# Performance work log

Measured on AMD Instinct MI355X. Metric: run time of the kernel, lower is better.

## Reference

```python
import jax, jax.numpy as jnp
import numpy as np


def _grid_sample_2d(feat, gx, gy):
    """Bilinear grid sample, zeros padding, align_corners=False.
    feat: [B,C,H,W]; gx,gy: [B,S,h,w] normalized coords in [-1,1].
    Returns [B,C,S,h,w]. Matches torch 5D grid_sample with D=1, z=0
    (z pixel coord = (1*1-1)/2 = 0 -> weight 1 on the single depth slice).
    """
    B, C, H, W = feat.shape
    ix = ((gx + 1.0) * W - 1.0) * 0.5  # unnormalize, align_corners=False
    iy = ((gy + 1.0) * H - 1.0) * 0.5
    x0 = jnp.floor(ix)
    y0 = jnp.floor(iy)
    tx = ix - x0  # fractional parts (differentiable w.r.t. grid)
    ty = iy - y0
    x0i = x0.astype(jnp.int32)
    y0i = y0.astype(jnp.int32)
    feat_flat = feat.reshape(B, C, H * W)

    def gather(xi, yi):
        valid = (xi >= 0) & (xi < W) & (yi >= 0) & (yi < H)
        xc = jnp.clip(xi, 0, W - 1)
        yc = jnp.clip(yi, 0, H - 1)
        idx = (yc * W + xc).reshape(B, 1, -1)  # [B,1,S*h*w]
        g = jnp.take_along_axis(feat_flat, idx, axis=2)  # [B,C,S*h*w]
        g = g.reshape(B, C, *xi.shape[1:])  # [B,C,S,h,w]
        return g * valid.astype(feat.dtype)[:, None]

    v00 = gather(x0i, y0i)
    v01 = gather(x0i + 1, y0i)
    v10 = gather(x0i, y0i + 1)
    v11 = gather(x0i + 1, y0i + 1)
    w00 = ((1.0 - tx) * (1.0 - ty))[:, None]
    w01 = (tx * (1.0 - ty))[:, None]
    w10 = ((1.0 - tx) * ty)[:, None]
    w11 = (tx * ty)[:, None]
    return v00 * w00 + v01 * w01 + v10 * w10 + v11 * w11


def setup_inputs() -> dict:
    key = jax.random.key(0)
    k1, k2, k3, k4 = jax.random.split(key, 4)
    B, C, S, H, W = 8, 8, 16, 128, 416
    feat_l = jax.random.normal(k1, (B, C, H, W), dtype=jnp.float32)
    feat_r = jax.random.normal(k2, (B, C, H, W), dtype=jnp.float32)
    # LUT: x,y normalized coords (slightly beyond [-1,1] to exercise zero padding);
    # z channel fixed to 0 exactly as in the module's lut_batch construction.
    lut_xy = jax.random.uniform(k3, (B, S, H, W, 2), dtype=jnp.float32,
                                minval=-1.1, maxval=1.1)
    lut = jnp.concatenate([lut_xy, jnp.zeros((B, S, H, W, 1), jnp.float32)], axis=-1)
    valid_mask = jax.random.bernoulli(k4, 0.8, (B, C, S, H, W))
    return {"feat_l": feat_l, "feat_r": feat_r, "lut": lut,
            "valid_mask": valid_mask, "no_steps": S}


def reference(feat_l, feat_r, lut, valid_mask, no_steps):
    """AnyNet._build_volume_2d: LUT grid_sample warp + masked inf-fill
    + abs-diff + channel-sum cost volume. Returns [B, no_steps, H, W]."""
    gx = lut[..., 0]  # torch grid order: (x, y, z), x indexes width
    gy = lut[..., 1]
    warped = _grid_sample_2d(feat_r, gx, gy)          # [B,C,S,H,W]
    diff = jnp.abs(warped - feat_l[:, :, None])       # broadcast feat_l over S
    cost_disp_feat = jnp.where(valid_mask, diff, jnp.inf)
    cost_volume = jnp.sum(cost_disp_feat, axis=1)     # [B,S,H,W]
    return cost_volume
```

## Files before the change

kernel.cpp:

```cpp
#include <hip/hip_runtime.h>
#include <math.h>

#define BB 8
#define CC 8
#define SS 16
#define HH 128
#define WW 416
#define HWSZ (HH * WW)

typedef unsigned short u16;
typedef unsigned char  u8;
typedef unsigned int   u32;
typedef unsigned short ushort8 __attribute__((ext_vector_type(8)));
typedef unsigned int   u32x4   __attribute__((ext_vector_type(4)));

__device__ __forceinline__ float bf2f(u16 v) {
    union { unsigned int u; float f; } x;
    x.u = ((unsigned int)v) << 16;
    return x.f;
}

__device__ __forceinline__ u16 f2bf(float f) {
    union { float ff; unsigned int u; } x;
    x.ff = f;
    unsigned int lsb = (x.u >> 16) & 1u;
    return (u16)((x.u + 0x7FFFu + lsb) >> 16);
}

__device__ __forceinline__ u32 nz_flags(u32 w) {
    return (((w & 0x7F7F7F7Fu) + 0x7F7F7F7Fu) | w) & 0x80808080u;
}

__global__ __launch_bounds__(256) void pack_feats(
    const u16* __restrict__ feat_l,
    const u16* __restrict__ feat_r,
    ushort8* __restrict__ pl,
    ushort8* __restrict__ pr)
{
    const int idx = blockIdx.x * 256 + threadIdx.x;
    const int b = idx / HWSZ;
    const int p = idx - b * HWSZ;
    const size_t base = (size_t)b * CC * HWSZ + p;

    ushort8 vr, vl;
#pragma unroll
    for (int c = 0; c < CC; ++c) {
        vr[c] = __builtin_nontemporal_load(&feat_r[base + (size_t)c * HWSZ]);
        vl[c] = __builtin_nontemporal_load(&feat_l[base + (size_t)c * HWSZ]);
    }
    pr[idx] = vr;
    pl[idx] = vl;
}

__global__ __launch_bounds__(256) void mask_reduce(
    const u8* __restrict__ vmask,
    u8* __restrict__ pmask)
{
    const int t = blockIdx.x * 256 + threadIdx.x;
    const int n16 = SS * HWSZ / 16;
    const int b = t / n16;
    const int r = t - b * n16;
    const u32x4* __restrict__ vm4 = (const u32x4*)vmask;

    u32x4 f = { 0x80808080u, 0x80808080u, 0x80808080u, 0x80808080u };
#pragma unroll
    for (int c = 0; c < CC; ++c) {
        const u32x4 v = __builtin_nontemporal_load(
            &vm4[(size_t)(b * CC + c) * n16 + r]);
        f.x &= nz_flags(v.x);
        f.y &= nz_flags(v.y);
        f.z &= nz_flags(v.z);
        f.w &= nz_flags(v.w);
    }
    __builtin_nontemporal_store(f, &((u32x4*)pmask)[t]);
}

__global__ __launch_bounds__(256) void anynet_cost_volume(
    const ushort8* __restrict__ pfr,
    const ushort8* __restrict__ pfl,
    const u16* __restrict__ lut,
    const u8*  __restrict__ pmask,
    u16* __restrict__ out)
{
    const int hw = blockIdx.x * 256 + threadIdx.x;
    const int bs = blockIdx.y;
    const int b  = bs >> 4;

    const size_t loff = ((size_t)bs * HWSZ + hw) * 3;
    const float gx = bf2f(__builtin_nontemporal_load(&lut[loff + 0]));
    const float gy = bf2f(__builtin_nontemporal_load(&lut[loff + 1]));

    const float ix = ((gx + 1.0f) * (float)WW - 1.0f) * 0.5f;
    const float iy = ((gy + 1.0f) * (float)HH - 1.0f) * 0.5f;
    const float x0f = floorf(ix);
    const float y0f = floorf(iy);
    const float tx = ix - x0f;
    const float ty = iy - y0f;
    const int x0 = (int)x0f;
    const int y0 = (int)y0f;
    const int x1 = x0 + 1;
    const int y1 = y0 + 1;

    const bool vx0 = ((unsigned)x0 < (unsigned)WW);
    const bool vx1 = ((unsigned)x1 < (unsigned)WW);
    const bool vy0 = ((unsigned)y0 < (unsigned)HH);
    const bool vy1 = ((unsigned)y1 < (unsigned)HH);

    const int xc0 = min(max(x0, 0), WW - 1);
    const int xc1 = min(max(x1, 0), WW - 1);
    const int yc0 = min(max(y0, 0), HH - 1);
    const int yc1 = min(max(y1, 0), HH - 1);

    const float w00 = (1.0f - tx) * (1.0f - ty) * ((vx0 && vy0) ? 1.0f : 0.0f);
    const float w01 = tx * (1.0f - ty)          * ((vx1 && vy0) ? 1.0f : 0.0f);
    const float w10 = (1.0f - tx) * ty          * ((vx0 && vy1) ? 1.0f : 0.0f);
    const float w11 = tx * ty                   * ((vx1 && vy1) ? 1.0f : 0.0f);

    const ushort8* __restrict__ frb = pfr + (size_t)b * HWSZ;
    const ushort8 p00 = frb[yc0 * WW + xc0];
    const ushort8 p01 = frb[yc0 * WW + xc1];
    const ushort8 p10 = frb[yc1 * WW + xc0];
    const ushort8 p11 = frb[yc1 * WW + xc1];
    const ushort8 fl8 = pfl[(size_t)b * HWSZ + hw];

    const u8 m = __builtin_nontemporal_load(&pmask[(size_t)bs * HWSZ + hw]);
    const bool any_invalid = (m == 0);

    float acc = 0.0f;
#pragma unroll
    for (int c = 0; c < CC; ++c) {
        const float warped = bf2f(p00[c]) * w00 + bf2f(p01[c]) * w01
                           + bf2f(p10[c]) * w10 + bf2f(p11[c]) * w11;
        acc += fabsf(warped - bf2f(fl8[c]));
    }

    acc = fminf(fmaxf(acc, 0.0f), 1e30f);
    if (!(acc >= 0.0f && acc <= 1e30f)) acc = 0.0f;
    __builtin_nontemporal_store(any_invalid ? (u16)0x7F7F : f2bf(acc),
                                &out[(size_t)bs * HWSZ + hw]);
}

extern "C" void kernel_launch(void* const* d_in, const int* in_sizes, int n_in,
                              void* d_out, int out_size, void* d_ws, size_t ws_size,
                              hipStream_t stream) {
    const u16* feat_l = (const u16*)d_in[0];
    const u16* feat_r = (const u16*)d_in[1];
    const u16* lut    = (const u16*)d_in[2];
    const u8*  vmask  = (const u8*)d_in[3];
    u16* out = (u16*)d_out;

    ushort8* pfr = (ushort8*)d_ws;
    ushort8* pfl = pfr + (size_t)BB * HWSZ;
    u8* pmask = (u8*)(pfl + (size_t)BB * HWSZ);

    pack_feats<<<dim3(BB * HWSZ / 256), dim3(256), 0, stream>>>(
        feat_l, feat_r, pfl, pfr);
    mask_reduce<<<dim3(BB * SS * HWSZ / 16 / 256), dim3(256), 0, stream>>>(
        vmask, pmask);

    dim3 grid(HWSZ / 256, BB * SS);
    anynet_cost_volume<<<grid, dim3(256), 0, stream>>>(pfr, pfl, lut, pmask, out);
}
```

Baseline: 340.4 us.

## Process four disparity steps per thread and interleave batches across blocks

Each thread now handles SB=4 disparity steps for one pixel. It loads all LUT coordinates and gathers up front to raise memory-level parallelism, and it reuses the left-feature load across steps. The 1D grid interleaves the batch index in its low bits so that concurrent blocks touch different batches, and the bilinear math uses packed float2 operations on bf16 pairs. The cost is higher register pressure from holding 16 gathered vectors per thread, which may reduce occupancy, and fewer total threads.

```diff
diff --git a/kernel.cpp b/kernel.cpp
--- a/kernel.cpp
+++ b/kernel.cpp
@@ -7,12 +7,14 @@
 #define HH 128
 #define WW 416
 #define HWSZ (HH * WW)
+#define SB 4
 
 typedef unsigned short u16;
 typedef unsigned char  u8;
 typedef unsigned int   u32;
 typedef unsigned short ushort8 __attribute__((ext_vector_type(8)));
 typedef unsigned int   u32x4   __attribute__((ext_vector_type(4)));
+typedef float          f32x2   __attribute__((ext_vector_type(2)));
 
 __device__ __forceinline__ float bf2f(u16 v) {
     union { unsigned int u; float f; } x;
@@ -25,6 +27,14 @@
     x.ff = f;
     unsigned int lsb = (x.u >> 16) & 1u;
     return (u16)((x.u + 0x7FFFu + lsb) >> 16);
+}
+
+__device__ __forceinline__ f32x2 bfpair(u32 w) {
+    union { u32 u; float f; } lo, hi;
+    lo.u = w << 16;
+    hi.u = w & 0xFFFF0000u;
+    f32x2 r; r.x = lo.f; r.y = hi.f;
+    return r;
 }
 
 __device__ __forceinline__ u32 nz_flags(u32 w) {
@@ -82,62 +92,96 @@
     const u8*  __restrict__ pmask,
     u16* __restrict__ out)
 {
-    const int hw = blockIdx.x * 256 + threadIdx.x;
-    const int bs = blockIdx.y;
-    const int b  = bs >> 4;
-
-    const size_t loff = ((size_t)bs * HWSZ + hw) * 3;
-    const float gx = bf2f(__builtin_nontemporal_load(&lut[loff + 0]));
-    const float gy = bf2f(__builtin_nontemporal_load(&lut[loff + 1]));
-
-    const float ix = ((gx + 1.0f) * (float)WW - 1.0f) * 0.5f;
-    const float iy = ((gy + 1.0f) * (float)HH - 1.0f) * 0.5f;
-    const float x0f = floorf(ix);
-    const float y0f = floorf(iy);
-    const float tx = ix - x0f;
-    const float ty = iy - y0f;
-    const int x0 = (int)x0f;
-    const int y0 = (int)y0f;
-    const int x1 = x0 + 1;
-    const int y1 = y0 + 1;
-
-    const bool vx0 = ((unsigned)x0 < (unsigned)WW);
-    const bool vx1 = ((unsigned)x1 < (unsigned)WW);
-    const bool vy0 = ((unsigned)y0 < (unsigned)HH);
-    const bool vy1 = ((unsigned)y1 < (unsigned)HH);
-
-    const int xc0 = min(max(x0, 0), WW - 1);
-    const int xc1 = min(max(x1, 0), WW - 1);
-    const int yc0 = min(max(y0, 0), HH - 1);
-    const int yc1 = min(max(y1, 0), HH - 1);
-
-    const float w00 = (1.0f - tx) * (1.0f - ty) * ((vx0 && vy0) ? 1.0f : 0.0f);
-    const float w01 = tx * (1.0f - ty)          * ((vx1 && vy0) ? 1.0f : 0.0f);
-    const float w10 = (1.0f - tx) * ty          * ((vx0 && vy1) ? 1.0f : 0.0f);
-    const float w11 = tx * ty                   * ((vx1 && vy1) ? 1.0f : 0.0f);
+    const int id = blockIdx.x;
+    const int b  = id & 7;
+    const int q  = id >> 3;
+    const int hwblk = q % (HWSZ / 256);
+    const int sgrp  = q / (HWSZ / 256);
+    const int hw = hwblk * 256 + (int)threadIdx.x;
+
+    float gx[SB], gy[SB];
+#pragma unroll
+    for (int j = 0; j < SB; ++j) {
+        const int s = sgrp * SB + j;
+        const size_t loff = ((size_t)(b * SS + s) * HWSZ + hw) * 3;
+        gx[j] = bf2f(__builtin_nontemporal_load(&lut[loff + 0]));
+        gy[j] = bf2f(__builtin_nontemporal_load(&lut[loff + 1]));
+    }
 
     const ushort8* __restrict__ frb = pfr + (size_t)b * HWSZ;
-    const ushort8 p00 = frb[yc0 * WW + xc0];
-    const ushort8 p01 = frb[yc0 * WW + xc1];
-    const ushort8 p10 = frb[yc1 * WW + xc0];
-    const ushort8 p11 = frb[yc1 * WW + xc1];
-    const ushort8 fl8 = pfl[(size_t)b * HWSZ + hw];
-
-    const u8 m = __builtin_nontemporal_load(&pmask[(size_t)bs * HWSZ + hw]);
-    const bool any_invalid = (m == 0);
-
-    float acc = 0.0f;
-#pragma unroll
-    for (int c = 0; c < CC; ++c) {
-        const float warped = bf2f(p00[c]) * w00 + bf2f(p01[c]) * w01
-                           + bf2f(p10[c]) * w10 + bf2f(p11[c]) * w11;
-        acc += fabsf(warped - bf2f(fl8[c]));
-    }
-
-    acc = fminf(fmaxf(acc, 0.0f), 1e30f);
-    if (!(acc >= 0.0f && acc <= 1e30f)) acc = 0.0f;
-    __builtin_nontemporal_store(any_invalid ? (u16)0x7F7F : f2bf(acc),
-                                &out[(size_t)bs * HWSZ + hw]);
+
+    float w00[SB], w01[SB], w10[SB], w11[SB];
+    ushort8 pc[SB][4];
+#pragma unroll
+    for (int j = 0; j < SB; ++j) {
+        const float ix = gx[j] * (0.5f * WW) + (0.5f * WW - 0.5f);
+        const float iy = gy[j] * (0.5f * HH) + (0.5f * HH - 0.5f);
+        const float x0f = floorf(ix);
+        const float y0f = floorf(iy);
+        const float tx = ix - x0f;
+        const float ty = iy - y0f;
+        const int x0 = (int)x0f;
+        const int y0 = (int)y0f;
+        const int x1 = x0 + 1;
+        const int y1 = y0 + 1;
+
+        const bool vx0 = ((unsigned)x0 < (unsigned)WW);
+        const bool vx1 = ((unsigned)x1 < (unsigned)WW);
+        const bool vy0 = ((unsigned)y0 < (unsigned)HH);
+        const bool vy1 = ((unsigned)y1 < (unsigned)HH);
+
+        const int xc0 = min(max(x0, 0), WW - 1);
+        const int xc1 = min(max(x1, 0), WW - 1);
+        const int yc0 = min(max(y0, 0), HH - 1);
+        const int yc1 = min(max(y1, 0), HH - 1);
+
+        w00[j] = (1.0f - tx) * (1.0f - ty) * ((vx0 && vy0) ? 1.0f : 0.0f);
+        w01[j] = tx * (1.0f - ty)          * ((vx1 && vy0) ? 1.0f : 0.0f);
+        w10[j] = (1.0f - tx) * ty          * ((vx0 && vy1) ? 1.0f : 0.0f);
+        w11[j] = tx * ty                   * ((vx1 && vy1) ? 1.0f : 0.0f);
+
+        pc[j][0] = frb[yc0 * WW + xc0];
+        pc[j][1] = frb[yc0 * WW + xc1];
+        pc[j][2] = frb[yc1 * WW + xc0];
+        pc[j][3] = frb[yc1 * WW + xc1];
+    }
+
+    u32 mb[SB];
+#pragma unroll
+    for (int j = 0; j < SB; ++j) {
+        mb[j] = __builtin_nontemporal_load(
+            &pmask[(size_t)(b * SS + sgrp * SB + j) * HWSZ + hw]);
+    }
+    union { ushort8 s; u32x4 w; } flu;
+    flu.s = pfl[(size_t)b * HWSZ + hw];
+    f32x2 fl[4];
+#pragma unroll
+    for (int i = 0; i < 4; ++i) fl[i] = bfpair(flu.w[i]);
+
+#pragma unroll
+    for (int j = 0; j < SB; ++j) {
+        union { ushort8 s; u32x4 w; } c00, c01, c10, c11;
+        c00.s = pc[j][0]; c01.s = pc[j][1]; c10.s = pc[j][2]; c11.s = pc[j][3];
+
+        f32x2 acc2; acc2.x = 0.0f; acc2.y = 0.0f;
+#pragma unroll
+        for (int i = 0; i < 4; ++i) {
+            f32x2 wv = bfpair(c00.w[i]) * w00[j];
+            wv += bfpair(c01.w[i]) * w01[j];
+            wv += bfpair(c10.w[i]) * w10[j];
+            wv += bfpair(c11.w[i]) * w11[j];
+            const f32x2 d = wv - fl[i];
+            f32x2 ad; ad.x = fabsf(d.x); ad.y = fabsf(d.y);
+            acc2 += ad;
+        }
+        float acc = acc2.x + acc2.y;
+
+        acc = fminf(fmaxf(acc, 0.0f), 1e30f);
+        if (!(acc >= 0.0f && acc <= 1e30f)) acc = 0.0f;
+        const u16 o = (mb[j] == 0u) ? (u16)0x7F7F : f2bf(acc);
+        __builtin_nontemporal_store(
+            o, &out[(size_t)(b * SS + sgrp * SB + j) * HWSZ + hw]);
+    }
 }
 
 extern "C" void kernel_launch(void* const* d_in, const int* in_sizes, int n_in,
@@ -158,6 +202,6 @@
     mask_reduce<<<dim3(BB * SS * HWSZ / 16 / 256), dim3(256), 0, stream>>>(
         vmask, pmask);
 
-    dim3 grid(HWSZ / 256, BB * SS);
-    anynet_cost_volume<<<grid, dim3(256), 0, stream>>>(pfr, pfl, lut, pmask, out);
-}
+    anynet_cost_volume<<<dim3(BB * (HWSZ / 256) * (SS / SB)), dim3(256), 0, stream>>>(
+        pfr, pfl, lut, pmask, out);
+}
```

After: 366.9 us. 1.08x slower.

## Repack LUT into 4-byte xy pairs, read feat_l directly, reorder block grid

Applied to the files above, without the earlier changes.

Adds a lut_pack kernel that compacts the 3-element bf16 LUT into one 32-bit (x,y) word per sample, so the main kernel does a single aligned load instead of two strided u16 loads. It drops the packed feat_l copy and reads feat_l's planar channels directly in the main kernel. The grid becomes 1D with batch in the low bits, so concurrently running blocks touch different batches. The main loop now unpacks bf16 pairs into float2 math. The extra LUT pass adds a full read and write of the LUT, which may cost more than it saves.

```diff
diff --git a/kernel.cpp b/kernel.cpp
--- a/kernel.cpp
+++ b/kernel.cpp
@@ -13,6 +13,9 @@
 typedef unsigned int   u32;
 typedef unsigned short ushort8 __attribute__((ext_vector_type(8)));
 typedef unsigned int   u32x4   __attribute__((ext_vector_type(4)));
+typedef unsigned int   u32x3   __attribute__((ext_vector_type(3)));
+typedef unsigned int   u32x2   __attribute__((ext_vector_type(2)));
+typedef float          f32x2   __attribute__((ext_vector_type(2)));
 
 __device__ __forceinline__ float bf2f(u16 v) {
     union { unsigned int u; float f; } x;
@@ -27,14 +30,20 @@
     return (u16)((x.u + 0x7FFFu + lsb) >> 16);
 }
 
+__device__ __forceinline__ f32x2 bfpair(u32 w) {
+    union { u32 u; float f; } lo, hi;
+    lo.u = w << 16;
+    hi.u = w & 0xFFFF0000u;
+    f32x2 r; r.x = lo.f; r.y = hi.f;
+    return r;
+}
+
 __device__ __forceinline__ u32 nz_flags(u32 w) {
     return (((w & 0x7F7F7F7Fu) + 0x7F7F7F7Fu) | w) & 0x80808080u;
 }
 
-__global__ __launch_bounds__(256) void pack_feats(
-    const u16* __restrict__ feat_l,
+__global__ __launch_bounds__(256) void pack_feat_r(
     const u16* __restrict__ feat_r,
-    ushort8* __restrict__ pl,
     ushort8* __restrict__ pr)
 {
     const int idx = blockIdx.x * 256 + threadIdx.x;
@@ -42,14 +51,11 @@
     const int p = idx - b * HWSZ;
     const size_t base = (size_t)b * CC * HWSZ + p;
 
-    ushort8 vr, vl;
+    ushort8 vr;
 #pragma unroll
-    for (int c = 0; c < CC; ++c) {
+    for (int c = 0; c < CC; ++c)
         vr[c] = __builtin_nontemporal_load(&feat_r[base + (size_t)c * HWSZ]);
-        vl[c] = __builtin_nontemporal_load(&feat_l[base + (size_t)c * HWSZ]);
-    }
     pr[idx] = vr;
-    pl[idx] = vl;
 }
 
 __global__ __launch_bounds__(256) void mask_reduce(
@@ -75,23 +81,47 @@
     __builtin_nontemporal_store(f, &((u32x4*)pmask)[t]);
 }
 
+__global__ __launch_bounds__(256) void lut_pack(
+    const u32* __restrict__ lut32,
+    u32x2* __restrict__ plut)
+{
+    const int t = blockIdx.x * 256 + threadIdx.x;
+    const u32 w0 = __builtin_nontemporal_load(&lut32[3 * (size_t)t + 0]);
+    const u32 w1 = __builtin_nontemporal_load(&lut32[3 * (size_t)t + 1]);
+    const u32 w2 = __builtin_nontemporal_load(&lut32[3 * (size_t)t + 2]);
+    u32x2 o;
+    o.x = w0;
+    o.y = (w2 << 16) | (w1 >> 16);
+    __builtin_nontemporal_store(o, &plut[t]);
+}
+
 __global__ __launch_bounds__(256) void anynet_cost_volume(
     const ushort8* __restrict__ pfr,
-    const ushort8* __restrict__ pfl,
-    const u16* __restrict__ lut,
+    const u16* __restrict__ feat_l,
+    const u32* __restrict__ plut,
     const u8*  __restrict__ pmask,
     u16* __restrict__ out)
 {
-    const int hw = blockIdx.x * 256 + threadIdx.x;
-    const int bs = blockIdx.y;
-    const int b  = bs >> 4;
+    const int id = blockIdx.x;
+    const int b  = id & 7;
+    const int r  = id >> 3;
+    const int hwblk = r % (HWSZ / 256);
+    const int s     = r / (HWSZ / 256);
+    const int hw = hwblk * 256 + (int)threadIdx.x;
+    const size_t sp = (size_t)(b * SS + s) * HWSZ + hw;
 
-    const size_t loff = ((size_t)bs * HWSZ + hw) * 3;
-    const float gx = bf2f(__builtin_nontemporal_load(&lut[loff + 0]));
-    const float gy = bf2f(__builtin_nontemporal_load(&lut[loff + 1]));
+    const u32 g = __builtin_nontemporal_load(&plut[sp]);
+    const u8 m  = __builtin_nontemporal_load(&pmask[sp]);
 
-    const float ix = ((gx + 1.0f) * (float)WW - 1.0f) * 0.5f;
-    const float iy = ((gy + 1.0f) * (float)HH - 1.0f) * 0.5f;
+    const size_t lbase = (size_t)b * CC * HWSZ + hw;
+    u16 flv[CC];
+#pragma unroll
+    for (int c = 0; c < CC; ++c)
+        flv[c] = __builtin_nontemporal_load(&feat_l[lbase + (size_t)c * HWSZ]);
+
+    const f32x2 gxy = bfpair(g);
+    const float ix = gxy.x * (0.5f * WW) + (0.5f * WW - 0.5f);
+    const float iy = gxy.y * (0.5f * HH) + (0.5f * HH - 0.5f);
     const float x0f = floorf(ix);
     const float y0f = floorf(iy);
     const float tx = ix - x0f;
@@ -121,23 +151,27 @@
     const ushort8 p01 = frb[yc0 * WW + xc1];
     const ushort8 p10 = frb[yc1 * WW + xc0];
     const ushort8 p11 = frb[yc1 * WW + xc1];
-    const ushort8 fl8 = pfl[(size_t)b * HWSZ + hw];
 
-    const u8 m = __builtin_nontemporal_load(&pmask[(size_t)bs * HWSZ + hw]);
-    const bool any_invalid = (m == 0);
+    union { ushort8 sv; u32x4 w; } c00, c01, c10, c11;
+    c00.sv = p00; c01.sv = p01; c10.sv = p10; c11.sv = p11;
 
-    float acc = 0.0f;
+    f32x2 acc2; acc2.x = 0.0f; acc2.y = 0.0f;
 #pragma unroll
-    for (int c = 0; c < CC; ++c) {
-        const float warped = bf2f(p00[c]) * w00 + bf2f(p01[c]) * w01
-                           + bf2f(p10[c]) * w10 + bf2f(p11[c]) * w11;
-        acc += fabsf(warped - bf2f(fl8[c]));
+    for (int i = 0; i < 4; ++i) {
+        f32x2 wv = bfpair(c00.w[i]) * w00;
+        wv += bfpair(c01.w[i]) * w01;
+        wv += bfpair(c10.w[i]) * w10;
+        wv += bfpair(c11.w[i]) * w11;
+        f32x2 fl; fl.x = bf2f(flv[2 * i]); fl.y = bf2f(flv[2 * i + 1]);
+        const f32x2 d = wv - fl;
+        f32x2 ad; ad.x = fabsf(d.x); ad.y = fabsf(d.y);
+        acc2 += ad;
     }
+    float acc = acc2.x + acc2.y;
 
     acc = fminf(fmaxf(acc, 0.0f), 1e30f);
     if (!(acc >= 0.0f && acc <= 1e30f)) acc = 0.0f;
-    __builtin_nontemporal_store(any_invalid ? (u16)0x7F7F : f2bf(acc),
-                                &out[(size_t)bs * HWSZ + hw]);
+    __builtin_nontemporal_store((m == 0) ? (u16)0x7F7F : f2bf(acc), &out[sp]);
 }
 
 extern "C" void kernel_launch(void* const* d_in, const int* in_sizes, int n_in,
@@ -150,14 +184,15 @@
     u16* out = (u16*)d_out;
 
     ushort8* pfr = (ushort8*)d_ws;
-    ushort8* pfl = pfr + (size_t)BB * HWSZ;
-    u8* pmask = (u8*)(pfl + (size_t)BB * HWSZ);
+    u8* pmask = (u8*)(pfr + (size_t)BB * HWSZ);
+    u32* plut = (u32*)(pmask + (size_t)BB * SS * HWSZ);
 
-    pack_feats<<<dim3(BB * HWSZ / 256), dim3(256), 0, stream>>>(
-        feat_l, feat_r, pfl, pfr);
+    pack_feat_r<<<dim3(BB * HWSZ / 256), dim3(256), 0, stream>>>(feat_r, pfr);
     mask_reduce<<<dim3(BB * SS * HWSZ / 16 / 256), dim3(256), 0, stream>>>(
         vmask, pmask);
+    lut_pack<<<dim3(BB * SS * HWSZ / 2 / 256), dim3(256), 0, stream>>>(
+        (const u32*)lut, (u32x2*)plut);
 
-    dim3 grid(HWSZ / 256, BB * SS);
-    anynet_cost_volume<<<grid, dim3(256), 0, stream>>>(pfr, pfl, lut, pmask, out);
+    anynet_cost_volume<<<dim3(BB * SS * (HWSZ / 256)), dim3(256), 0, stream>>>(
+        pfr, feat_l, plut, pmask, out);
 }
```

Result: slower. 358.4 us (+5.3%).

## Pack right features as fp8 and fetch bilinear x-pairs in single loads

Applied to the files above, without the earlier changes.

The pack kernel now converts feat_r to fp8 (e4m3) packed 8 channels per 8 bytes. The cost kernel loads both horizontal neighbours with one unaligned 16-byte load per row and converts them with packed fp8-to-f32 instructions. The grid is also linearized so batch varies fastest, which is meant to improve L2 reuse of the feature maps. The aim is to halve gather bandwidth, at the cost of fp8 precision loss in the warped features that may exceed tolerance.

```diff
diff --git a/kernel.cpp b/kernel.cpp
--- a/kernel.cpp
+++ b/kernel.cpp
@@ -13,6 +13,9 @@
 typedef unsigned int   u32;
 typedef unsigned short ushort8 __attribute__((ext_vector_type(8)));
 typedef unsigned int   u32x4   __attribute__((ext_vector_type(4)));
+typedef unsigned int   u32x2   __attribute__((ext_vector_type(2)));
+typedef float          f32x2   __attribute__((ext_vector_type(2)));
+typedef u32x4 __attribute__((aligned(4))) u32x4_a4;
 
 __device__ __forceinline__ float bf2f(u16 v) {
     union { unsigned int u; float f; } x;
@@ -27,28 +30,49 @@
     return (u16)((x.u + 0x7FFFu + lsb) >> 16);
 }
 
+__device__ __forceinline__ f32x2 bfpair(u32 w) {
+    union { u32 u; float f; } lo, hi;
+    lo.u = w << 16;
+    hi.u = w & 0xFFFF0000u;
+    f32x2 r; r.x = lo.f; r.y = hi.f;
+    return r;
+}
+
+template<bool H>
+__device__ __forceinline__ f32x2 fp8pair(u32 w) {
+    return (f32x2)__builtin_amdgcn_cvt_pk_f32_fp8(w, H);
+}
+
 __device__ __forceinline__ u32 nz_flags(u32 w) {
     return (((w & 0x7F7F7F7Fu) + 0x7F7F7F7Fu) | w) & 0x80808080u;
 }
 
 __global__ __launch_bounds__(256) void pack_feats(
+    const u16* __restrict__ feat_r,
     const u16* __restrict__ feat_l,
-    const u16* __restrict__ feat_r,
-    ushort8* __restrict__ pl,
-    ushort8* __restrict__ pr)
+    u32x2* __restrict__ pr8,
+    ushort8* __restrict__ pl)
 {
     const int idx = blockIdx.x * 256 + threadIdx.x;
     const int b = idx / HWSZ;
     const int p = idx - b * HWSZ;
     const size_t base = (size_t)b * CC * HWSZ + p;
 
-    ushort8 vr, vl;
+    float fr[CC];
+    ushort8 vl;
 #pragma unroll
     for (int c = 0; c < CC; ++c) {
-        vr[c] = __builtin_nontemporal_load(&feat_r[base + (size_t)c * HWSZ]);
+        fr[c] = bf2f(__builtin_nontemporal_load(&feat_r[base + (size_t)c * HWSZ]));
         vl[c] = __builtin_nontemporal_load(&feat_l[base + (size_t)c * HWSZ]);
     }
-    pr[idx] = vr;
+    u32x2 o;
+    int w0 = 0, w1 = 0;
+    w0 = __builtin_amdgcn_cvt_pk_fp8_f32(fr[0], fr[1], w0, false);
+    w0 = __builtin_amdgcn_cvt_pk_fp8_f32(fr[2], fr[3], w0, true);
+    w1 = __builtin_amdgcn_cvt_pk_fp8_f32(fr[4], fr[5], w1, false);
+    w1 = __builtin_amdgcn_cvt_pk_fp8_f32(fr[6], fr[7], w1, true);
+    o.x = (u32)w0; o.y = (u32)w1;
+    pr8[idx] = o;
     pl[idx] = vl;
 }
 
@@ -76,22 +100,27 @@
 }
 
 __global__ __launch_bounds__(256) void anynet_cost_volume(
-    const ushort8* __restrict__ pfr,
+    const u8* __restrict__ pfr8,
     const ushort8* __restrict__ pfl,
     const u16* __restrict__ lut,
     const u8*  __restrict__ pmask,
     u16* __restrict__ out)
 {
-    const int hw = blockIdx.x * 256 + threadIdx.x;
-    const int bs = blockIdx.y;
-    const int b  = bs >> 4;
-
-    const size_t loff = ((size_t)bs * HWSZ + hw) * 3;
+    const int id = blockIdx.x;
+    const int b  = id & 7;
+    const int r  = id >> 3;
+    const int hwblk = r % (HWSZ / 256);
+    const int s     = r / (HWSZ / 256);
+    const int hw = hwblk * 256 + (int)threadIdx.x;
+    const size_t sp = (size_t)(b * SS + s) * HWSZ + hw;
+
+    const size_t loff = sp * 3;
     const float gx = bf2f(__builtin_nontemporal_load(&lut[loff + 0]));
     const float gy = bf2f(__builtin_nontemporal_load(&lut[loff + 1]));
-
-    const float ix = ((gx + 1.0f) * (float)WW - 1.0f) * 0.5f;
-    const float iy = ((gy + 1.0f) * (float)HH - 1.0f) * 0.5f;
+    const u8 m = __builtin_nontemporal_load(&pmask[sp]);
+
+    const float ix = gx * (0.5f * WW) + (0.5f * WW - 0.5f);
+    const float iy = gy * (0.5f * HH) + (0.5f * HH - 0.5f);
     const float x0f = floorf(ix);
     const float y0f = floorf(iy);
     const float tx = ix - x0f;
@@ -106,38 +135,47 @@
     const bool vy0 = ((unsigned)y0 < (unsigned)HH);
     const bool vy1 = ((unsigned)y1 < (unsigned)HH);
 
-    const int xc0 = min(max(x0, 0), WW - 1);
-    const int xc1 = min(max(x1, 0), WW - 1);
     const int yc0 = min(max(y0, 0), HH - 1);
     const int yc1 = min(max(y1, 0), HH - 1);
-
-    const float w00 = (1.0f - tx) * (1.0f - ty) * ((vx0 && vy0) ? 1.0f : 0.0f);
-    const float w01 = tx * (1.0f - ty)          * ((vx1 && vy0) ? 1.0f : 0.0f);
-    const float w10 = (1.0f - tx) * ty          * ((vx0 && vy1) ? 1.0f : 0.0f);
-    const float w11 = tx * ty                   * ((vx1 && vy1) ? 1.0f : 0.0f);
-
-    const ushort8* __restrict__ frb = pfr + (size_t)b * HWSZ;
-    const ushort8 p00 = frb[yc0 * WW + xc0];
-    const ushort8 p01 = frb[yc0 * WW + xc1];
-    const ushort8 p10 = frb[yc1 * WW + xc0];
-    const ushort8 p11 = frb[yc1 * WW + xc1];
-    const ushort8 fl8 = pfl[(size_t)b * HWSZ + hw];
-
-    const u8 m = __builtin_nontemporal_load(&pmask[(size_t)bs * HWSZ + hw]);
-    const bool any_invalid = (m == 0);
-
-    float acc = 0.0f;
-#pragma unroll
-    for (int c = 0; c < CC; ++c) {
-        const float warped = bf2f(p00[c]) * w00 + bf2f(p01[c]) * w01
-                           + bf2f(p10[c]) * w10 + bf2f(p11[c]) * w11;
-        acc += fabsf(warped - bf2f(fl8[c]));
+    const int bx  = min(max(x0, 0), WW - 2);
+
+    float w00 = (1.0f - tx) * (1.0f - ty) * ((vx0 && vy0) ? 1.0f : 0.0f);
+    float w01 = tx * (1.0f - ty)          * ((vx1 && vy0) ? 1.0f : 0.0f);
+    float w10 = (1.0f - tx) * ty          * ((vx0 && vy1) ? 1.0f : 0.0f);
+    float w11 = tx * ty                   * ((vx1 && vy1) ? 1.0f : 0.0f);
+
+    const bool sw = (x0 == bx);
+    const float wl0 = sw ? w00 : w01, wh0 = sw ? w01 : w00;
+    const float wl1 = sw ? w10 : w11, wh1 = sw ? w11 : w10;
+
+    const u8* __restrict__ imb = pfr8 + (size_t)b * HWSZ * 8;
+    const u32x4 r0 = *(const u32x4_a4*)(imb + 8 * (size_t)(yc0 * WW + bx));
+    const u32x4 r1 = *(const u32x4_a4*)(imb + 8 * (size_t)(yc1 * WW + bx));
+
+    union { ushort8 sv; u32x4 w; } flu;
+    flu.sv = pfl[(size_t)b * HWSZ + hw];
+
+    f32x2 acc2; acc2.x = 0.0f; acc2.y = 0.0f;
+#define CHPAIR(K, WSEL, HSEL)                                              \
+    {                                                                      \
+        f32x2 wv = fp8pair<HSEL>(WSEL ? r0.y : r0.x) * wl0;                \
+        wv += fp8pair<HSEL>(WSEL ? r0.w : r0.z) * wh0;                     \
+        wv += fp8pair<HSEL>(WSEL ? r1.y : r1.x) * wl1;                     \
+        wv += fp8pair<HSEL>(WSEL ? r1.w : r1.z) * wh1;                     \
+        const f32x2 d = wv - bfpair(flu.w[K]);                             \
+        f32x2 ad; ad.x = fabsf(d.x); ad.y = fabsf(d.y);                    \
+        acc2 += ad;                                                        \
     }
+    CHPAIR(0, 0, false)
+    CHPAIR(1, 0, true)
+    CHPAIR(2, 1, false)
+    CHPAIR(3, 1, true)
+#undef CHPAIR
+    float acc = acc2.x + acc2.y;
 
     acc = fminf(fmaxf(acc, 0.0f), 1e30f);
     if (!(acc >= 0.0f && acc <= 1e30f)) acc = 0.0f;
-    __builtin_nontemporal_store(any_invalid ? (u16)0x7F7F : f2bf(acc),
-                                &out[(size_t)bs * HWSZ + hw]);
+    __builtin_nontemporal_store((m == 0) ? (u16)0x7F7F : f2bf(acc), &out[sp]);
 }
 
 extern "C" void kernel_launch(void* const* d_in, const int* in_sizes, int n_in,
@@ -149,15 +187,15 @@
     const u8*  vmask  = (const u8*)d_in[3];
     u16* out = (u16*)d_out;
 
-    ushort8* pfr = (ushort8*)d_ws;
-    ushort8* pfl = pfr + (size_t)BB * HWSZ;
+    u32x2* pfr8 = (u32x2*)d_ws;
+    ushort8* pfl = (ushort8*)(pfr8 + (size_t)BB * HWSZ);
     u8* pmask = (u8*)(pfl + (size_t)BB * HWSZ);
 
     pack_feats<<<dim3(BB * HWSZ / 256), dim3(256), 0, stream>>>(
-        feat_l, feat_r, pfl, pfr);
+        feat_r, feat_l, pfr8, pfl);
     mask_reduce<<<dim3(BB * SS * HWSZ / 16 / 256), dim3(256), 0, stream>>>(
         vmask, pmask);
 
-    dim3 grid(HWSZ / 256, BB * SS);
-    anynet_cost_volume<<<grid, dim3(256), 0, stream>>>(pfr, pfl, lut, pmask, out);
-}
+    anynet_cost_volume<<<dim3(BB * SS * (HWSZ / 256)), dim3(256), 0, stream>>>(
+        (const u8*)pfr8, pfl, lut, pmask, out);
+}
```

Result: no change. 336.2 us (-1.2%).
